# Kernel optimization log

Measured on AMD Instinct MI355X. Metric: run time of the kernel, lower is better.

The kernel has to match this reference:

```python
import jax, jax.numpy as jnp
import numpy as np
import math

D_MODEL = 512
N_HEADS = 8
D_K = D_MODEL // N_HEADS
B, S, KC = 16, 1024, 32
NEG = -1e32


def setup_inputs() -> dict:
    key = jax.random.key(0)
    ks = jax.random.split(key, 14)
    s = 1.0 / math.sqrt(D_MODEL)
    return {
        "q": jax.random.normal(ks[0], (B, S, D_MODEL), jnp.float32),
        "k": jax.random.normal(ks[1], (B, S, D_MODEL), jnp.float32),
        "v": jax.random.normal(ks[2], (B, S, D_MODEL), jnp.float32),
        "q_seq": jax.random.randint(ks[3], (B, S), 0, 500, jnp.int32),
        "c_seq": jax.random.randint(ks[4], (B, S, KC), 0, 2, jnp.int32),
        "Wq": jax.random.normal(ks[5], (D_MODEL, D_MODEL), jnp.float32) * s,
        "bq": jnp.zeros((D_MODEL,), jnp.float32),
        "Wk": jax.random.normal(ks[6], (D_MODEL, D_MODEL), jnp.float32) * s,
        "bk": jnp.zeros((D_MODEL,), jnp.float32),
        "Wv": jax.random.normal(ks[7], (D_MODEL, D_MODEL), jnp.float32) * s,
        "bv": jnp.zeros((D_MODEL,), jnp.float32),
        "Wo": jax.random.normal(ks[8], (D_MODEL, D_MODEL), jnp.float32) * s,
        "bo": jnp.zeros((D_MODEL,), jnp.float32),
    }


def qc_mask(q_seq, c_seq):
    # maskq[b,i,j] = 1 if same question id
    maskq = (q_seq[:, :, None] == q_seq[:, None, :]).astype(jnp.int32)
    # maskc[b,i,j] = 1 if any shared concept; entries are {0,1} so AND-sum == dot
    overlap = jnp.einsum("bik,bjk->bij", c_seq, c_seq)  # int32
    maskc = (overlap > 0).astype(jnp.int32)
    # strict lower triangle: 1 - triu(ones, k=0)
    tri = jnp.tril(jnp.ones((S, S), jnp.int32), k=-1)[None]
    return (maskc + maskq + 1) * tri  # values in {0,1,2,3}


def reference(q, k, v, q_seq, c_seq, Wq, bq, Wk, bk, Wv, bv, Wo, bo):
    bs = q.shape[0]
    # NOTE: original code swaps the linears: k<-k_linear(k), q<-v_linear(q), v<-q_linear(v)
    kh = (k @ Wk.T + bk).reshape(bs, S, N_HEADS, D_K).transpose(0, 2, 1, 3)
    qh = (q @ Wv.T + bv).reshape(bs, S, N_HEADS, D_K).transpose(0, 2, 1, 3)
    vh = (v @ Wq.T + bq).reshape(bs, S, N_HEADS, D_K).transpose(0, 2, 1, 3)

    mask = qc_mask(q_seq, c_seq)  # [B,S,S] int
    scores = jnp.einsum("bhid,bhjd->bhij", qh, kh) / math.sqrt(D_K)
    m = mask[:, None]  # [B,1,S,S]
    scores = jnp.where(m == 0, NEG, scores)
    scores = jax.nn.softmax(scores, axis=-1)

    adjustments = jnp.array([0.0, 0.5, 1.0, 2.0], jnp.float32)
    adjusted = scores * adjustments[m]
    sums = jnp.sum(scores, axis=-1, keepdims=True)
    sums = jnp.where(sums == 0, jnp.ones_like(sums), sums)
    adjusted = adjusted / sums

    out = jnp.einsum("bhij,bhjd->bhid", adjusted, vh)
    concat = out.transpose(0, 2, 1, 3).reshape(bs, S, D_MODEL)
    return concat @ Wo.T + bo
```

## Files before the change

kernel.cpp:

```cpp
#include <hip/hip_runtime.h>
#include <stdint.h>

typedef unsigned short u16;
typedef unsigned int   u32;
typedef unsigned long long u64;
typedef __attribute__((ext_vector_type(8)))  short short8;
typedef __attribute__((ext_vector_type(4)))  float f32x4;
typedef __attribute__((ext_vector_type(16))) float f32x16;
typedef __attribute__((ext_vector_type(4)))  unsigned int u32x4;

__device__ __forceinline__ u16 f2bf(float f) {
  u32 u = __builtin_bit_cast(u32, f);
  u32 r = u + 0x7FFFu + ((u >> 16) & 1u);
  return (u16)(r >> 16);
}

__device__ __forceinline__ u32 cvtpk(float a, float b) {
  u32 r;
  asm("v_cvt_pk_bf16_f32 %0, %1, %2" : "=v"(r) : "v"(a), "v"(b));
  return r;
}

__device__ __forceinline__ void gload_lds16(const void* g, void* l) {
  __builtin_amdgcn_global_load_lds(
      (__attribute__((address_space(1))) void*)(uintptr_t)g,
      (__attribute__((address_space(3))) void*)(u32)(uintptr_t)l,
      16, 0, 0);
}

#define SB() __builtin_amdgcn_sched_barrier(0)

__global__ void cast4_kernel(const float* __restrict__ s0, const float* __restrict__ s1,
                             const float* __restrict__ s2, const float* __restrict__ s3,
                             u16* __restrict__ d0, u16* __restrict__ d1,
                             u16* __restrict__ d2, u16* __restrict__ d3, int n8) {
  const int sel = blockIdx.y;
  const float* src = sel == 0 ? s0 : sel == 1 ? s1 : sel == 2 ? s2 : s3;
  u16* dst = sel == 0 ? d0 : sel == 1 ? d1 : sel == 2 ? d2 : d3;
  int i = blockIdx.x * blockDim.x + threadIdx.x;
  if (i >= n8) return;
  const float4* s4 = (const float4*)src;
  float4 x = s4[2 * (size_t)i];
  float4 y = s4[2 * (size_t)i + 1];
  u32x4 r;
  r.x = cvtpk(x.x, x.y); r.y = cvtpk(x.z, x.w);
  r.z = cvtpk(y.x, y.y); r.w = cvtpk(y.z, y.w);
  *(u32x4*)(dst + 8 * (size_t)i) = r;
}

__global__ void pack_kernel(const int* __restrict__ q_seq, const int* __restrict__ c_seq,
                            int2* __restrict__ meta, int n) {
  int i = blockIdx.x * blockDim.x + threadIdx.x;
  if (i >= n) return;
  u32 bits = 0;
#pragma unroll
  for (int j = 0; j < 32; ++j)
    bits |= (c_seq[(size_t)i * 32 + j] != 0) ? (1u << j) : 0u;
  meta[i] = make_int2(q_seq[i], (int)bits);
}

__global__ __launch_bounds__(256) void mask_kernel(const int2* __restrict__ meta,
                                                   u64* __restrict__ maskw) {
  const int qc = blockIdx.x, kt = blockIdx.y, b = blockIdx.z;
  const int t = threadIdx.x;
  const int q = qc * 256 + t;
  __shared__ int2 colm[32];
  if (t < 32) colm[t] = meta[b * 1024 + kt * 32 + t];
  __syncthreads();
  const int2 qm = meta[b * 1024 + q];
  const int rs = qm.x; const u32 rb = (u32)qm.y;
  u64 w = 0;
#pragma unroll
  for (int j = 0; j < 32; ++j) {
    const int2 cm = colm[j];
    const int kj = kt * 32 + j;
    u32 m = 0;
    if (kj < q) m = 1u + (rs == cm.x ? 1u : 0u) + (((rb & (u32)cm.y) != 0u) ? 1u : 0u);
    w |= (u64)m << (2 * j);
  }
  maskw[((size_t)b * 32 + kt) * 1024 + q] = w;
}

__global__ __launch_bounds__(256) void gemm_qkv(const float* __restrict__ qf,
                                                const float* __restrict__ kf,
                                                const float* __restrict__ vf,
                                                const u16* __restrict__ Wcat,
                                                const float* __restrict__ bv,
                                                const float* __restrict__ bk,
                                                const float* __restrict__ bq,
                                                u16* __restrict__ qhb,
                                                u16* __restrict__ khb,
                                                u16* __restrict__ vTb,
                                                float kscale) {
  const int K = 512;
  __shared__ __align__(16) u16 As[128 * 64];
  __shared__ __align__(16) u16 Bs[2][128 * 64];
  const int t    = threadIdx.x;
  const int lane = t & 63;
  const int wid  = t >> 6;
  const int g    = lane >> 4, l15 = lane & 15;
  const int wm   = wid >> 1, wn = wid & 1;
  const int wrk  = (blockIdx.x & 7) * 192 + (blockIdx.x >> 3);
  const int mb   = wrk >> 2, nbi = wrk & 3;
  const int which = mb >> 7;
  const float* Ax   = which == 0 ? qf : which == 1 ? kf : vf;
  const float* bias = which == 0 ? bv : which == 1 ? bk : bq;
  const float scale = which == 1 ? kscale : 1.0f;
  u16* outb = which == 0 ? qhb : which == 1 ? khb : vTb;
  const int mloc = (mb & 127) << 7;
  const int n0   = nbi << 7;
  const u16* W   = Wcat + (size_t)which * 512 * 512;

  const int srow = t >> 3;
  const int scol = (((t & 7) ^ (srow & 7)) << 3);
  const int dcol = ((t & 7) << 3);
  const int rsw  = l15 & 7;

  f32x4 acc[4][4];
#pragma unroll
  for (int i = 0; i < 4; ++i)
#pragma unroll
    for (int j = 0; j < 4; ++j) acc[i][j] = f32x4{0.f, 0.f, 0.f, 0.f};

  float4 ax[4], ay[4];

#define LOAD_A(kt)                                                            \
  {                                                                           \
    _Pragma("unroll")                                                         \
    for (int i = 0; i < 4; ++i) {                                             \
      const float* src = Ax + (size_t)(mloc + 32 * i + srow) * K + (kt) * 64 + scol; \
      ax[i] = *(const float4*)src;                                            \
      ay[i] = *(const float4*)(src + 4);                                      \
    }                                                                         \
  }
#define STAGE_B(kt, buf)                                                      \
  {                                                                           \
    _Pragma("unroll")                                                         \
    for (int i = 0; i < 4; ++i)                                               \
      gload_lds16(W + (size_t)(n0 + i * 32 + srow) * K + (kt) * 64 + scol,    \
                  &Bs[buf][i * 2048 + t * 8]);                                \
  }
#define WRITE_A()                                                             \
  {                                                                           \
    _Pragma("unroll")                                                         \
    for (int i = 0; i < 4; ++i) {                                             \
      u32x4 r;                                                                \
      r.x = cvtpk(ax[i].x, ax[i].y); r.y = cvtpk(ax[i].z, ax[i].w);           \
      r.z = cvtpk(ay[i].x, ay[i].y); r.w = cvtpk(ay[i].z, ay[i].w);           \
      *(u32x4*)(&As[(32 * i + srow) * 64 + dcol]) = r;                        \
    }                                                                         \
  }
#define COMPUTE(buf)                                                          \
  {                                                                           \
    _Pragma("unroll")                                                         \
    for (int kk = 0; kk < 2; ++kk) {                                          \
      short8 a[4], b[4];                                                      \
      _Pragma("unroll")                                                       \
      for (int mi = 0; mi < 4; ++mi)                                          \
        a[mi] = *(const short8*)(&As[(wm * 64 + mi * 16 + l15) * 64           \
                                 + (((kk * 4 + g) ^ rsw) << 3)]);             \
      _Pragma("unroll")                                                       \
      for (int ni = 0; ni < 4; ++ni)                                          \
        b[ni] = *(const short8*)(&Bs[buf][(wn * 64 + ni * 16 + l15) * 64      \
                                 + (((kk * 4 + g) ^ rsw) << 3)]);             \
      _Pragma("unroll")                                                       \
      for (int mi = 0; mi < 4; ++mi)                                          \
        _Pragma("unroll")                                                     \
        for (int ni = 0; ni < 4; ++ni)                                        \
          acc[mi][ni] = __builtin_amdgcn_mfma_f32_16x16x32_bf16(a[mi], b[ni], acc[mi][ni], 0, 0, 0); \
    }                                                                         \
  }

  LOAD_A(0); SB();
  STAGE_B(0, 0); SB();

  for (int tt = 0; tt < 8; ++tt) {
    const int cur = tt & 1, nxt = cur ^ 1;
    asm volatile("s_waitcnt vmcnt(4)" ::: "memory");
    SB();
    WRITE_A();
    SB();
    const int kn = (tt + 1) & 7;
    LOAD_A(kn); SB();
    STAGE_B(kn, nxt); SB();
    asm volatile("s_waitcnt vmcnt(12) lgkmcnt(0)" ::: "memory");
    __builtin_amdgcn_s_barrier();
    SB();
    COMPUTE(cur);
    SB();
    __builtin_amdgcn_s_barrier();
    SB();
  }
  asm volatile("s_waitcnt vmcnt(0)" ::: "memory");

#undef LOAD_A
#undef STAGE_B
#undef WRITE_A
#undef COMPUTE

#pragma unroll
  for (int ni = 0; ni < 4; ++ni) {
    const int col = n0 + wn * 64 + ni * 16 + l15;
    const float bz = bias[col];
#pragma unroll
    for (int mi = 0; mi < 4; ++mi) {
#pragma unroll
      for (int r = 0; r < 4; ++r) {
        const int row = mloc + wm * 64 + mi * 16 + g * 4 + r;
        const u16 val = f2bf((acc[mi][ni][r] + bz) * scale);
        const size_t base = ((size_t)(row >> 10) * 8 + (col >> 6)) * 65536;
        const int s = row & 1023, d = col & 63;
        if (which == 0) {
          outb[base + (size_t)s * 64 + d] = val;
        } else if (which == 1) {
          outb[base + (s >> 5) * 2048 + (d >> 3) * 256 + (s & 31) * 8 + (d & 7)] = val;
        } else {
          outb[base + (s >> 3) * 512 + d * 8 + (s & 7)] = val;
        }
      }
    }
  }
}

__global__ __launch_bounds__(256) void gemm_out(const u16* __restrict__ A,
                                                const u16* __restrict__ W,
                                                const float* __restrict__ bias,
                                                float* __restrict__ outp) {
  const int K = 512, N = 512;
  __shared__ __align__(16) u16 As[2][128 * 64];
  __shared__ __align__(16) u16 Bs[2][128 * 64];
  const int t    = threadIdx.x;
  const int lane = t & 63;
  const int wid  = t >> 6;
  const int g    = lane >> 4, l15 = lane & 15;
  const int wm   = wid >> 1, wn = wid & 1;
  const int wrk  = (blockIdx.x & 7) * 64 + (blockIdx.x >> 3);
  const int mb   = wrk >> 2, nbi = wrk & 3;
  const int m0   = mb << 7, n0 = nbi << 7;
  const int srow = t >> 3;
  const int scol = (((t & 7) ^ (srow & 7)) << 3);
  const int rsw  = l15 & 7;

  f32x4 acc[4][4];
#pragma unroll
  for (int i = 0; i < 4; ++i)
#pragma unroll
    for (int j = 0; j < 4; ++j) acc[i][j] = f32x4{0.f, 0.f, 0.f, 0.f};

#define STAGE(kt, buf)                                                        \
  {                                                                           \
    _Pragma("unroll")                                                         \
    for (int i = 0; i < 4; ++i) {                                             \
      gload_lds16(A + (size_t)(m0 + i * 32 + srow) * K + (kt) * 64 + scol,    \
                  &As[buf][i * 2048 + t * 8]);                                \
      gload_lds16(W + (size_t)(n0 + i * 32 + srow) * K + (kt) * 64 + scol,    \
                  &Bs[buf][i * 2048 + t * 8]);                                \
    }                                                                         \
  }
#define COMPUTE(buf)                                                          \
  {                                                                           \
    _Pragma("unroll")                                                         \
    for (int kk = 0; kk < 2; ++kk) {                                          \
      short8 a[4], b[4];                                                      \
      _Pragma("unroll")                                                       \
      for (int mi = 0; mi < 4; ++mi)                                          \
        a[mi] = *(const short8*)(&As[buf][(wm * 64 + mi * 16 + l15) * 64      \
                                 + (((kk * 4 + g) ^ rsw) << 3)]);             \
      _Pragma("unroll")                                                       \
      for (int ni = 0; ni < 4; ++ni)                                          \
        b[ni] = *(const short8*)(&Bs[buf][(wn * 64 + ni * 16 + l15) * 64      \
                                 + (((kk * 4 + g) ^ rsw) << 3)]);             \
      _Pragma("unroll")                                                       \
      for (int mi = 0; mi < 4; ++mi)                                          \
        _Pragma("unroll")                                                     \
        for (int ni = 0; ni < 4; ++ni)                                        \
          acc[mi][ni] = __builtin_amdgcn_mfma_f32_16x16x32_bf16(a[mi], b[ni], acc[mi][ni], 0, 0, 0); \
    }                                                                         \
  }

  STAGE(0, 0); SB();
  for (int tt = 0; tt < 8; ++tt) {
    const int cur = tt & 1, nxt = cur ^ 1;
    STAGE((tt + 1) & 7, nxt); SB();
    asm volatile("s_waitcnt vmcnt(8)" ::: "memory");
    __builtin_amdgcn_s_barrier();
    SB();
    COMPUTE(cur);
    SB();
    __builtin_amdgcn_s_barrier();
    SB();
  }
  asm volatile("s_waitcnt vmcnt(0)" ::: "memory");
#undef STAGE
#undef COMPUTE

#pragma unroll
  for (int ni = 0; ni < 4; ++ni) {
    const int col = n0 + wn * 64 + ni * 16 + l15;
    const float bz = bias[col];
#pragma unroll
    for (int mi = 0; mi < 4; ++mi)
#pragma unroll
      for (int r = 0; r < 4; ++r) {
        const int row = m0 + wm * 64 + mi * 16 + g * 4 + r;
        outp[(size_t)row * N + col] = acc[mi][ni][r] + bz;
      }
  }
}

__global__ __launch_bounds__(256, 4) void attn_kernel(const u16* __restrict__ qh,
                                                      const u16* __restrict__ kh,
                                                      const u16* __restrict__ vT,
                                                      const u64* __restrict__ maskw,
                                                      u16* __restrict__ outc) {
  const int h  = blockIdx.x;
  const int qp = blockIdx.y;
  const int b  = blockIdx.z;
  const int lane = threadIdx.x & 63;
  const int wid  = threadIdx.x >> 6;
  const int pair = wid >> 1, p = wid & 1;
  const int l31 = lane & 31;
  const int hh  = lane >> 5;
  const int hh8 = hh << 3, fourh = hh << 2, eighth = hh << 3;
  const int jt = pair ? (31 - qp) : qp;
  const int q0 = jt << 5;
  const int qi = q0 + l31;
  const size_t bh = (size_t)b * 8 + h;
  const u16* Q  = qh + bh * 65536;
  const u16* Kp = kh + bh * 65536;
  const u16* Vt = vT + bh * 65536;
  const u64* mrow = maskw + (size_t)b * 32768 + qi;

  __shared__ float mO[2][32][64];
  __shared__ float mL[2][64];
  __shared__ __align__(16) float Sl[2][32];

  short8 qB[4];
#pragma unroll
  for (int i = 0; i < 4; ++i)
    qB[i] = *(const short8*)(Q + (size_t)qi * 64 + i * 16 + eighth);

  f32x16 O0, O1;
#pragma unroll
  for (int i = 0; i < 16; ++i) { O0[i] = 0.f; O1[i] = 0.f; }
  float lr[4] = {0.f, 0.f, 0.f, 0.f};

  const int nt = jt + 1;

  short8 kA[4];
#pragma unroll
  for (int i = 0; i < 4; ++i)
    kA[i] = *(const short8*)(Kp + p * 2048 + ((2 * i + hh) * 32 + l31) * 8);
  u64 wm = mrow[(size_t)p << 10];

  for (int t = p; t < nt; t += 2) {
    const int k0 = t << 5;

    f32x16 S;
#pragma unroll
    for (int i = 0; i < 16; ++i) S[i] = 0.f;
#pragma unroll
    for (int i = 0; i < 4; ++i)
      S = __builtin_amdgcn_mfma_f32_32x32x16_bf16(kA[i], qB[i], S, 0, 0, 0);

    u64 wmn = 0;
    if (t + 2 < nt) {
#pragma unroll
      for (int i = 0; i < 4; ++i)
        kA[i] = *(const short8*)(Kp + (t + 2) * 2048 + ((2 * i + hh) * 32 + l31) * 8);
      wmn = mrow[(size_t)(t + 2) << 10];
    }

    short8 vB[2][2];
#pragma unroll
    for (int t4 = 0; t4 < 2; ++t4)
#pragma unroll
      for (int j = 0; j < 2; ++j)
        vB[t4][j] = *(const short8*)(Vt + (size_t)(t * 4 + t4 * 2 + hh) * 512 + (32 * j + l31) * 8);

    const u32 wsh0 = ((u32)wm) >> hh8;
    const u32 wsh1 = ((u32)(wm >> 32)) >> hh8;
    u32 pk[8];
#pragma unroll
    for (int s = 0; s < 4; ++s) {
      const u32 wsel = (s < 2) ? wsh0 : wsh1;
      float pv[4];
#pragma unroll
      for (int r = 0; r < 4; ++r) {
        const int m = 4 * s + r;
        const u32 m2 = (wsel >> (2 * r + 16 * (s & 1))) & 3u;
        float e;
        asm("v_exp_f32 %0, %1" : "=v"(e) : "v"(S[m]));
        const float pp = (m2 != 0u) ? e : 0.f;
        lr[r] += pp;
        asm("v_ldexp_f32 %0, %1, %2" : "=v"(pv[r]) : "v"(pp), "v"(m2));
      }
      pk[2 * s]     = cvtpk(pv[0], pv[1]);
      pk[2 * s + 1] = cvtpk(pv[2], pv[3]);
    }
    wm = wmn;

#pragma unroll
    for (int t4 = 0; t4 < 2; ++t4) {
      u32 a0 = pk[4 * t4 + 0], b0 = pk[4 * t4 + 2];
      u32 a1 = pk[4 * t4 + 1], b1 = pk[4 * t4 + 3];
      asm("v_permlane32_swap_b32 %0, %1" : "+v"(a0), "+v"(b0));
      asm("v_permlane32_swap_b32 %0, %1" : "+v"(a1), "+v"(b1));
      u32x4 w; w.x = a0; w.y = a1; w.z = b0; w.w = b1;
      const short8 pa = __builtin_bit_cast(short8, w);
      O0 = __builtin_amdgcn_mfma_f32_32x32x16_bf16(pa, vB[t4][0], O0, 0, 0, 0);
      O1 = __builtin_amdgcn_mfma_f32_32x32x16_bf16(pa, vB[t4][1], O1, 0, 0, 0);
    }
  }

  float lrun = (lr[0] + lr[1]) + (lr[2] + lr[3]);

  if (p == 1) {
#pragma unroll
    for (int r = 0; r < 16; ++r) {
      mO[pair][r][lane]      = O0[r];
      mO[pair][16 + r][lane] = O1[r];
    }
    mL[pair][lane] = lrun;
  }
  __syncthreads();
  if (p == 0) {
#pragma unroll
    for (int r = 0; r < 16; ++r) {
      O0[r] += mO[pair][r][lane];
      O1[r] += mO[pair][16 + r][lane];
    }
    lrun += mL[pair][lane];

    const float ssum = lrun + __shfl_xor(lrun, 32);
    if (lane < 32) Sl[pair][l31] = (ssum > 0.f) ? 0.25f / ssum : 0.f;
    __builtin_amdgcn_sched_barrier(0);
    asm volatile("s_waitcnt lgkmcnt(0)" ::: "memory");
    __builtin_amdgcn_sched_barrier(0);
#pragma unroll
    for (int t2 = 0; t2 < 4; ++t2) {
      const float4 inv4 = *(const float4*)&Sl[pair][8 * t2 + fourh];
#pragma unroll
      for (int r = 0; r < 4; ++r) {
        const int m = 4 * t2 + r;
        const float iv = (r == 0) ? inv4.x : (r == 1) ? inv4.y : (r == 2) ? inv4.z : inv4.w;
        const int qrow = q0 + 8 * t2 + fourh + r;
        u16* op = outc + ((size_t)b * 1024 + qrow) * 512 + h * 64;
        op[l31]      = f2bf(O0[m] * iv);
        op[32 + l31] = f2bf(O1[m] * iv);
      }
    }
  }
}

extern "C" void kernel_launch(void* const* d_in, const int* in_sizes, int n_in,
                              void* d_out, int out_size, void* d_ws, size_t ws_size,
                              hipStream_t stream) {
  (void)in_sizes; (void)n_in; (void)out_size; (void)ws_size;
  const float* q    = (const float*)d_in[0];
  const float* k    = (const float*)d_in[1];
  const float* v    = (const float*)d_in[2];
  const int*  q_seq = (const int*)d_in[3];
  const int*  c_seq = (const int*)d_in[4];
  const float* Wq   = (const float*)d_in[5];
  const float* bq   = (const float*)d_in[6];
  const float* Wk   = (const float*)d_in[7];
  const float* bk   = (const float*)d_in[8];
  const float* Wv   = (const float*)d_in[9];
  const float* bv   = (const float*)d_in[10];
  const float* Wo   = (const float*)d_in[11];
  const float* bo   = (const float*)d_in[12];
  float* out = (float*)d_out;

  char* ws = (char*)d_ws;
  const size_t SZH = 16ull * 8 * 1024 * 64 * 2;
  u16* qhb   = (u16*)(ws + 0 * SZH);
  u16* khb   = (u16*)(ws + 1 * SZH);
  u16* vTb   = (u16*)(ws + 2 * SZH);
  u16* attnc = (u16*)(ws + 3 * SZH);
  u16* Wvb = (u16*)(ws + 4 * SZH + 0 * 524288);
  u16* Wkb = (u16*)(ws + 4 * SZH + 1 * 524288);
  u16* Wqb = (u16*)(ws + 4 * SZH + 2 * 524288);
  u16* Wob = (u16*)(ws + 4 * SZH + 3 * 524288);
  int2* meta  = (int2*)(ws + 4 * SZH + 4 * 524288);
  u64* maskw  = (u64*)(ws + 4 * SZH + 4 * 524288 + 131072);

  const int n8w = 512 * 512 / 8;
  cast4_kernel<<<dim3(n8w / 256, 4), 256, 0, stream>>>(Wv, Wk, Wq, Wo,
                                                       Wvb, Wkb, Wqb, Wob, n8w);
  pack_kernel<<<64, 256, 0, stream>>>(q_seq, c_seq, meta, 16384);
  mask_kernel<<<dim3(4, 32, 16), 256, 0, stream>>>(meta, maskw);

  const float KSCALE = 0.18033688011112042f;
  gemm_qkv<<<dim3(1536), 256, 0, stream>>>(q, k, v, Wvb, bv, bk, bq,
                                           qhb, khb, vTb, KSCALE);
  attn_kernel<<<dim3(8, 16, 16), 256, 0, stream>>>(qhb, khb, vTb, maskw, attnc);
  gemm_out<<<512, 256, 0, stream>>>(attnc, Wob, bo, out);
}
```

Baseline: 144.4 us.

## Keep full-K A row block resident in LDS and sweep all N tiles

The QKV projection now gives each block a 64-row slab of the fp32 activations. It converts the whole K=512 slab to bf16 in LDS once, then loops over all four 128-column N tiles, streaming weight tiles through registers into a single LDS buffer. Previously each activation element was loaded and converted once per N tile (four times). The change targets that redundant global traffic and conversion work. In exchange it uses a 64KB A buffer, halves the MFMA tile per block, adds two barriers per step, and loses the async global-to-LDS double buffering of B.

```diff
diff --git a/kernel.cpp b/kernel.cpp
--- a/kernel.cpp
+++ b/kernel.cpp
@@ -81,144 +81,126 @@
   maskw[((size_t)b * 32 + kt) * 1024 + q] = w;
 }
 
-__global__ __launch_bounds__(256) void gemm_qkv(const float* __restrict__ qf,
-                                                const float* __restrict__ kf,
-                                                const float* __restrict__ vf,
-                                                const u16* __restrict__ Wcat,
-                                                const float* __restrict__ bv,
-                                                const float* __restrict__ bk,
-                                                const float* __restrict__ bq,
-                                                u16* __restrict__ qhb,
-                                                u16* __restrict__ khb,
-                                                u16* __restrict__ vTb,
-                                                float kscale) {
+__global__ __launch_bounds__(256, 2) void gemm_qkv(const float* __restrict__ qf,
+                                                   const float* __restrict__ kf,
+                                                   const float* __restrict__ vf,
+                                                   const u16* __restrict__ Wcat,
+                                                   const float* __restrict__ bv,
+                                                   const float* __restrict__ bk,
+                                                   const float* __restrict__ bq,
+                                                   u16* __restrict__ qhb,
+                                                   u16* __restrict__ khb,
+                                                   u16* __restrict__ vTb,
+                                                   float kscale) {
   const int K = 512;
-  __shared__ __align__(16) u16 As[128 * 64];
-  __shared__ __align__(16) u16 Bs[2][128 * 64];
+  __shared__ __align__(16) u16 Albs[64 * 512];
+  __shared__ __align__(16) u16 Bbuf[128 * 64];
   const int t    = threadIdx.x;
   const int lane = t & 63;
   const int wid  = t >> 6;
   const int g    = lane >> 4, l15 = lane & 15;
   const int wm   = wid >> 1, wn = wid & 1;
-  const int wrk  = (blockIdx.x & 7) * 192 + (blockIdx.x >> 3);
-  const int mb   = wrk >> 2, nbi = wrk & 3;
-  const int which = mb >> 7;
+  const int mb   = (blockIdx.x & 7) * 96 + (blockIdx.x >> 3);
+  const int which = mb >> 8;
   const float* Ax   = which == 0 ? qf : which == 1 ? kf : vf;
   const float* bias = which == 0 ? bv : which == 1 ? bk : bq;
   const float scale = which == 1 ? kscale : 1.0f;
   u16* outb = which == 0 ? qhb : which == 1 ? khb : vTb;
-  const int mloc = (mb & 127) << 7;
-  const int n0   = nbi << 7;
+  const int mloc = (mb & 255) << 6;
   const u16* W   = Wcat + (size_t)which * 512 * 512;
 
   const int srow = t >> 3;
   const int scol = (((t & 7) ^ (srow & 7)) << 3);
-  const int dcol = ((t & 7) << 3);
   const int rsw  = l15 & 7;
 
-  f32x4 acc[4][4];
+#pragma unroll
+  for (int j = 0; j < 16; ++j) {
+    const int u = j * 256 + t;
+    const int row = u >> 6;
+    const int slot = u & 63;
+    const float* src = Ax + (size_t)(mloc + row) * K + slot * 8;
+    const float4 x = *(const float4*)src;
+    const float4 y = *(const float4*)(src + 4);
+    u32x4 r;
+    r.x = cvtpk(x.x, x.y); r.y = cvtpk(x.z, x.w);
+    r.z = cvtpk(y.x, y.y); r.w = cvtpk(y.z, y.w);
+    *(u32x4*)(&Albs[row * 512 + ((slot ^ (row & 7)) << 3)]) = r;
+  }
+
+  short8 breg[4];
 #pragma unroll
   for (int i = 0; i < 4; ++i)
+    breg[i] = *(const short8*)(W + (size_t)(i * 32 + srow) * K + scol);
+#pragma unroll
+  for (int i = 0; i < 4; ++i)
+    *(short8*)(&Bbuf[i * 2048 + t * 8]) = breg[i];
+  __syncthreads();
+
+  f32x4 acc[2][4];
+#pragma unroll
+  for (int i = 0; i < 2; ++i)
 #pragma unroll
     for (int j = 0; j < 4; ++j) acc[i][j] = f32x4{0.f, 0.f, 0.f, 0.f};
 
-  float4 ax[4], ay[4];
-
-#define LOAD_A(kt)                                                            \
-  {                                                                           \
-    _Pragma("unroll")                                                         \
-    for (int i = 0; i < 4; ++i) {                                             \
-      const float* src = Ax + (size_t)(mloc + 32 * i + srow) * K + (kt) * 64 + scol; \
-      ax[i] = *(const float4*)src;                                            \
-      ay[i] = *(const float4*)(src + 4);                                      \
-    }                                                                         \
-  }
-#define STAGE_B(kt, buf)                                                      \
-  {                                                                           \
-    _Pragma("unroll")                                                         \
-    for (int i = 0; i < 4; ++i)                                               \
-      gload_lds16(W + (size_t)(n0 + i * 32 + srow) * K + (kt) * 64 + scol,    \
-                  &Bs[buf][i * 2048 + t * 8]);                                \
-  }
-#define WRITE_A()                                                             \
-  {                                                                           \
-    _Pragma("unroll")                                                         \
-    for (int i = 0; i < 4; ++i) {                                             \
-      u32x4 r;                                                                \
-      r.x = cvtpk(ax[i].x, ax[i].y); r.y = cvtpk(ax[i].z, ax[i].w);           \
-      r.z = cvtpk(ay[i].x, ay[i].y); r.w = cvtpk(ay[i].z, ay[i].w);           \
-      *(u32x4*)(&As[(32 * i + srow) * 64 + dcol]) = r;                        \
-    }                                                                         \
-  }
-#define COMPUTE(buf)                                                          \
-  {                                                                           \
-    _Pragma("unroll")                                                         \
-    for (int kk = 0; kk < 2; ++kk) {                                          \
-      short8 a[4], b[4];                                                      \
-      _Pragma("unroll")                                                       \
-      for (int mi = 0; mi < 4; ++mi)                                          \
-        a[mi] = *(const short8*)(&As[(wm * 64 + mi * 16 + l15) * 64           \
-                                 + (((kk * 4 + g) ^ rsw) << 3)]);             \
-      _Pragma("unroll")                                                       \
-      for (int ni = 0; ni < 4; ++ni)                                          \
-        b[ni] = *(const short8*)(&Bs[buf][(wn * 64 + ni * 16 + l15) * 64      \
-                                 + (((kk * 4 + g) ^ rsw) << 3)]);             \
-      _Pragma("unroll")                                                       \
-      for (int mi = 0; mi < 4; ++mi)                                          \
-        _Pragma("unroll")                                                     \
-        for (int ni = 0; ni < 4; ++ni)                                        \
-          acc[mi][ni] = __builtin_amdgcn_mfma_f32_16x16x32_bf16(a[mi], b[ni], acc[mi][ni], 0, 0, 0); \
-    }                                                                         \
-  }
-
-  LOAD_A(0); SB();
-  STAGE_B(0, 0); SB();
-
-  for (int tt = 0; tt < 8; ++tt) {
-    const int cur = tt & 1, nxt = cur ^ 1;
-    asm volatile("s_waitcnt vmcnt(4)" ::: "memory");
+  for (int s = 0; s < 32; ++s) {
+    const int sn = (s + 1) & 31;
+    const int nbn = sn >> 3, ksn = sn & 7;
+#pragma unroll
+    for (int i = 0; i < 4; ++i)
+      breg[i] = *(const short8*)(W + (size_t)(nbn * 128 + i * 32 + srow) * K
+                                 + ksn * 64 + scol);
     SB();
-    WRITE_A();
-    SB();
-    const int kn = (tt + 1) & 7;
-    LOAD_A(kn); SB();
-    STAGE_B(kn, nxt); SB();
-    asm volatile("s_waitcnt vmcnt(12) lgkmcnt(0)" ::: "memory");
-    __builtin_amdgcn_s_barrier();
-    SB();
-    COMPUTE(cur);
-    SB();
-    __builtin_amdgcn_s_barrier();
-    SB();
-  }
-  asm volatile("s_waitcnt vmcnt(0)" ::: "memory");
-
-#undef LOAD_A
-#undef STAGE_B
-#undef WRITE_A
-#undef COMPUTE
-
-#pragma unroll
-  for (int ni = 0; ni < 4; ++ni) {
-    const int col = n0 + wn * 64 + ni * 16 + l15;
-    const float bz = bias[col];
-#pragma unroll
-    for (int mi = 0; mi < 4; ++mi) {
-#pragma unroll
-      for (int r = 0; r < 4; ++r) {
-        const int row = mloc + wm * 64 + mi * 16 + g * 4 + r;
-        const u16 val = f2bf((acc[mi][ni][r] + bz) * scale);
-        const size_t base = ((size_t)(row >> 10) * 8 + (col >> 6)) * 65536;
-        const int s = row & 1023, d = col & 63;
-        if (which == 0) {
-          outb[base + (size_t)s * 64 + d] = val;
-        } else if (which == 1) {
-          outb[base + (s >> 5) * 2048 + (d >> 3) * 256 + (s & 31) * 8 + (d & 7)] = val;
-        } else {
-          outb[base + (s >> 3) * 512 + d * 8 + (s & 7)] = val;
+    const int ks = s & 7;
+#pragma unroll
+    for (int kk = 0; kk < 2; ++kk) {
+      const int slot = ks * 8 + kk * 4 + g;
+      short8 a[2], b[4];
+#pragma unroll
+      for (int mi = 0; mi < 2; ++mi) {
+        const int row = wm * 32 + mi * 16 + l15;
+        a[mi] = *(const short8*)(&Albs[row * 512 + ((slot ^ (row & 7)) << 3)]);
+      }
+#pragma unroll
+      for (int ni = 0; ni < 4; ++ni)
+        b[ni] = *(const short8*)(&Bbuf[(wn * 64 + ni * 16 + l15) * 64
+                                 + (((kk * 4 + g) ^ rsw) << 3)]);
+#pragma unroll
+      for (int mi = 0; mi < 2; ++mi)
+#pragma unroll
+        for (int ni = 0; ni < 4; ++ni)
+          acc[mi][ni] = __builtin_amdgcn_mfma_f32_16x16x32_bf16(a[mi], b[ni], acc[mi][ni], 0, 0, 0);
+    }
+    __syncthreads();
+#pragma unroll
+    for (int i = 0; i < 4; ++i)
+      *(short8*)(&Bbuf[i * 2048 + t * 8]) = breg[i];
+    if ((s & 7) == 7) {
+      const int nbi = s >> 3;
+#pragma unroll
+      for (int ni = 0; ni < 4; ++ni) {
+        const int col = nbi * 128 + wn * 64 + ni * 16 + l15;
+        const float bz = bias[col];
+#pragma unroll
+        for (int mi = 0; mi < 2; ++mi) {
+#pragma unroll
+          for (int r = 0; r < 4; ++r) {
+            const int row = mloc + wm * 32 + mi * 16 + g * 4 + r;
+            const u16 val = f2bf((acc[mi][ni][r] + bz) * scale);
+            const size_t base = ((size_t)(row >> 10) * 8 + (col >> 6)) * 65536;
+            const int ss = row & 1023, d = col & 63;
+            if (which == 0) {
+              outb[base + (size_t)ss * 64 + d] = val;
+            } else if (which == 1) {
+              outb[base + (ss >> 5) * 2048 + (d >> 3) * 256 + (ss & 31) * 8 + (d & 7)] = val;
+            } else {
+              outb[base + (ss >> 3) * 512 + d * 8 + (ss & 7)] = val;
+            }
+          }
+          acc[mi][ni] = f32x4{0.f, 0.f, 0.f, 0.f};
         }
       }
     }
+    __syncthreads();
   }
 }
 
@@ -492,8 +474,8 @@
   mask_kernel<<<dim3(4, 32, 16), 256, 0, stream>>>(meta, maskw);
 
   const float KSCALE = 0.18033688011112042f;
-  gemm_qkv<<<dim3(1536), 256, 0, stream>>>(q, k, v, Wvb, bv, bk, bq,
-                                           qhb, khb, vTb, KSCALE);
+  gemm_qkv<<<dim3(768), 256, 0, stream>>>(q, k, v, Wvb, bv, bk, bq,
+                                          qhb, khb, vTb, KSCALE);
   attn_kernel<<<dim3(8, 16, 16), 256, 0, stream>>>(qhb, khb, vTb, maskw, attnc);
   gemm_out<<<512, 256, 0, stream>>>(attnc, Wob, bo, out);
 }
```

New measurement: 157.3 us. 8.9% more time.
